# Optimization experiments

Measured on AMD Instinct MI355X. Metric: run time of the kernel, lower is better.

## Reference

```python
import jax, jax.numpy as jnp
import numpy as np

B, IN, OUT = 131072, 256, 256
BITWIDTH = 7.0


def setup_inputs() -> dict:
    key = jax.random.key(0)
    k1, k2 = jax.random.split(key)
    # simulated int8 activations (integer-valued float32)
    act_in = jax.random.randint(k1, (B, IN), -127, 128).astype(jnp.float32)
    # UniformWeights: xavier_uniform then weight_quant to the int8 grid
    limit = float(np.sqrt(6.0 / (IN + OUT)))
    w = jax.random.uniform(k2, (OUT, IN), minval=-limit, maxval=limit, dtype=jnp.float32)
    w_range = jnp.max(jnp.abs(w))
    weight_exp = (jnp.ceil(jnp.log2(w_range)) - 7.0).astype(jnp.int32)
    weight = jnp.round(w / w_range * 127.0)  # int8-valued float32 [OUT, IN]
    return {"act_in": act_in, "exp_in": jnp.int32(0), "weight": weight, "weight_exp": weight_exp}


def _round_shift(x, shift):
    # RoundShift: floor-div by 2**shift, add floor(|remainder| / 2**(shift-1)), clip to int8
    two_s = jnp.exp2(shift)
    rt = jnp.floor(x / two_s)
    prob = jnp.abs(x - rt * two_s)
    dec = jnp.floor(prob / jnp.exp2(shift - 1.0))
    return jnp.clip(rt + dec, -127.0, 127.0)


def reference(act_in, exp_in, weight, weight_exp):
    # int8 GEMM simulated in fp32 (exact: |acc| < 2^24)
    temp = act_in @ weight.T  # [B, OUT] int32 accumulator values
    # RangeEstimate: full-tensor abs-max -> bitwidth
    r = jnp.max(jnp.abs(temp))
    bw = jnp.where(r > 0, jnp.ceil(jnp.log2(jnp.maximum(r, 1.0))), 0.0)
    shift = bw - BITWIDTH
    pos = shift > 0
    safe_shift = jnp.maximum(shift, 1.0)
    rounded = _round_shift(temp, safe_shift)
    act_out = jnp.where(pos, rounded, temp).astype(jnp.int8)
    exp_sum = jnp.asarray(exp_in, jnp.int32) + jnp.asarray(weight_exp, jnp.int32)
    exp_out = (exp_sum + jnp.where(pos, shift, 0.0).astype(jnp.int32)).astype(jnp.int16)
    return act_out, exp_out
```

## Files before the change

### kernel.cpp

```cpp
#include <hip/hip_runtime.h>
#include <stdint.h>


#define M_ROWS 131072
#define NK 256
#define BM 64
#define BK 64
#define BKP 72

typedef __attribute__((ext_vector_type(8))) short bf16x8;
typedef __attribute__((ext_vector_type(4))) float f32x4;
typedef __attribute__((ext_vector_type(4))) float fv4;
typedef __attribute__((ext_vector_type(4))) int iv4;
typedef __attribute__((ext_vector_type(4))) unsigned int u32x4;
typedef __attribute__((ext_vector_type(4))) unsigned short us4;

__device__ __forceinline__ uint32_t pack_bf16(float a, float b) {
  return (__float_as_uint(a) >> 16) | (__float_as_uint(b) & 0xFFFF0000u);
}

__global__ void wconv(const float* __restrict__ w, unsigned short* __restrict__ wb,
                      int* __restrict__ gmax) {
  if (blockIdx.x == 0 && threadIdx.x == 0) *gmax = 0;
  const int i = blockIdx.x * 256 + threadIdx.x;
  const fv4 f = ((const fv4*)w)[i];
  us4 o;
  o.x = (unsigned short)(__float_as_uint(f.x) >> 16);
  o.y = (unsigned short)(__float_as_uint(f.y) >> 16);
  o.z = (unsigned short)(__float_as_uint(f.z) >> 16);
  o.w = (unsigned short)(__float_as_uint(f.w) >> 16);
  ((us4*)wb)[i] = o;
}

__device__ __forceinline__ void gemm_tile(
    const float* __restrict__ act, const unsigned short* __restrict__ wgtb,
    short* As, short* Bs, f32x4 acc[4][4])
{
  const int tid  = threadIdx.x;
  const int bm   = blockIdx.x * BM;
  const int lane = tid & 63;
  const int wave = tid >> 6;
  const int lm   = lane & 15;
  const int lk   = lane >> 4;
  const int wn   = wave * 64;

  const int arow = tid >> 3, aks = (tid & 7) * 8;
  const int brow = tid >> 3, bks = (tid & 7) * 8;

  uint32_t apk[2][4];
  u32x4 breg[8];

#pragma unroll
  for (int j = 0; j < 2; ++j) {
    const float* p = act + (size_t)(bm + arow + j * 32) * NK + aks;
    const fv4 f0 = *(const fv4*)p;
    const fv4 f1 = *((const fv4*)p + 1);
    apk[j][0] = pack_bf16(f0.x, f0.y); apk[j][1] = pack_bf16(f0.z, f0.w);
    apk[j][2] = pack_bf16(f1.x, f1.y); apk[j][3] = pack_bf16(f1.z, f1.w);
  }
#pragma unroll
  for (int j = 0; j < 8; ++j)
    breg[j] = *(const u32x4*)(wgtb + (size_t)(brow + j * 32) * NK + bks);

  for (int kt = 0; kt < NK; kt += BK) {
    __syncthreads();
#pragma unroll
    for (int j = 0; j < 2; ++j)
      *(u32x4*)&As[(arow + j * 32) * BKP + aks] = *(const u32x4*)apk[j];
#pragma unroll
    for (int j = 0; j < 8; ++j)
      *(u32x4*)&Bs[(brow + j * 32) * BKP + bks] = breg[j];
    __syncthreads();

    if (kt + BK < NK) {
      const int ktn = kt + BK;
#pragma unroll
      for (int j = 0; j < 2; ++j) {
        const float* p = act + (size_t)(bm + arow + j * 32) * NK + ktn + aks;
        const fv4 f0 = *(const fv4*)p;
        const fv4 f1 = *((const fv4*)p + 1);
        apk[j][0] = pack_bf16(f0.x, f0.y); apk[j][1] = pack_bf16(f0.z, f0.w);
        apk[j][2] = pack_bf16(f1.x, f1.y); apk[j][3] = pack_bf16(f1.z, f1.w);
      }
#pragma unroll
      for (int j = 0; j < 8; ++j)
        breg[j] = *(const u32x4*)(wgtb + (size_t)(brow + j * 32) * NK + ktn + bks);
    }

#pragma unroll
    for (int kk = 0; kk < BK; kk += 32) {
      bf16x8 af[4], bfr[4];
#pragma unroll
      for (int mi = 0; mi < 4; ++mi)
        af[mi] = *(const bf16x8*)&As[(mi * 16 + lm) * BKP + kk + lk * 8];
#pragma unroll
      for (int ni = 0; ni < 4; ++ni)
        bfr[ni] = *(const bf16x8*)&Bs[(wn + ni * 16 + lm) * BKP + kk + lk * 8];
#pragma unroll
      for (int mi = 0; mi < 4; ++mi)
#pragma unroll
        for (int ni = 0; ni < 4; ++ni)
          acc[mi][ni] = __builtin_amdgcn_mfma_f32_16x16x32_bf16(
              af[mi], bfr[ni], acc[mi][ni], 0, 0, 0);
    }
  }
}

__global__ __launch_bounds__(256, 3) void gemm_maxstore(
    const float* __restrict__ act, const unsigned short* __restrict__ wgtb,
    int* __restrict__ out, int* __restrict__ gmax)
{
  __shared__ __align__(16) short As[BM * BKP];
  __shared__ __align__(16) short Bs[NK * BKP];
  __shared__ int smax;
  const int tid = threadIdx.x;
  if (tid == 0) smax = 0;

  f32x4 acc[4][4] = {};
  gemm_tile(act, wgtb, As, Bs, acc);

  const int bm   = blockIdx.x * BM;
  const int lane = tid & 63;
  const int lm   = lane & 15;
  const int lk   = lane >> 4;
  const int wn   = (tid >> 6) * 64;

  int imax = 0;
#pragma unroll
  for (int mi = 0; mi < 4; ++mi)
#pragma unroll
    for (int ni = 0; ni < 4; ++ni)
#pragma unroll
      for (int r = 0; r < 4; ++r) {
        const int ti = (int)acc[mi][ni][r];
        const int a = ti < 0 ? -ti : ti;
        imax = a > imax ? a : imax;
        const int m = bm + mi * 16 + lk * 4 + r;
        const int n = wn + ni * 16 + lm;
        out[(size_t)m * NK + n] = ti;
      }
#pragma unroll
  for (int off = 32; off; off >>= 1) {
    const int o = __shfl_xor(imax, off, 64);
    imax = o > imax ? o : imax;
  }
  if ((tid & 63) == 0) atomicMax(&smax, imax);
  __syncthreads();
  if (tid == 0) atomicMax(gmax, smax);
}

__global__ __launch_bounds__(256) void quant_pass(
    int* __restrict__ out, const int* __restrict__ gmax,
    const int* __restrict__ exp_in, const int* __restrict__ wexp)
{
  const int rmax = *gmax;
  const int bw = (rmax <= 1) ? 0 : (32 - __clz(rmax - 1));
  const int shift = bw - 7;
  const bool pos = shift > 0;
  const int s = shift < 1 ? 1 : shift;

  const size_t total  = (size_t)M_ROWS * NK / 4;
  const size_t stride = (size_t)gridDim.x * blockDim.x;
  for (size_t i = (size_t)blockIdx.x * blockDim.x + threadIdx.x; i < total;
       i += stride) {
    iv4 t = ((const iv4*)out)[i];
    iv4 q;
#pragma unroll
    for (int j = 0; j < 4; ++j) {
      const int ti = t[j];
      int r;
      if (pos) {
        const int rt = ti >> s;
        const int dec = (ti - (rt << s)) >> (s - 1);
        r = rt + dec;
        r = r > 127 ? 127 : (r < -127 ? -127 : r);
      } else {
        r = (int)(signed char)(ti & 0xFF);
      }
      q[j] = r;
    }
    __builtin_nontemporal_store(q, &((iv4*)out)[i]);
  }

  if (blockIdx.x == 0 && threadIdx.x == 0) {
    const int e = exp_in[0] + wexp[0] + (pos ? shift : 0);
    out[(size_t)M_ROWS * NK] = (int)(short)e;
  }
}

extern "C" void kernel_launch(void* const* d_in, const int* in_sizes, int n_in,
                              void* d_out, int out_size, void* d_ws, size_t ws_size,
                              hipStream_t stream) {
  const float* act   = (const float*)d_in[0];
  const int* exp_in  = (const int*)d_in[1];
  const float* wgt   = (const float*)d_in[2];
  const int* wexp    = (const int*)d_in[3];
  int* gmax          = (int*)d_ws;
  unsigned short* wb = (unsigned short*)((char*)d_ws + 128);

  wconv<<<dim3(64), dim3(256), 0, stream>>>(wgt, wb, gmax);
  gemm_maxstore<<<dim3(M_ROWS / BM), dim3(256), 0, stream>>>(act, wb, (int*)d_out,
                                                             gmax);
  quant_pass<<<dim3(2048), dim3(256), 0, stream>>>((int*)d_out, gmax, exp_in, wexp);
}
```

Measured before the change: 280.2 us.

## Keep full weight matrix resident in LDS, stream activations directly into registers

The GEMM kernel now loads the entire bf16 weight matrix into shared memory once per block and uses 512-row blocks of 512 threads. Each wave computes 16-row strips over all 256 output columns, loading activation fragments straight from global memory into registers without staging them in LDS. This removes the per-k-tile barriers and the repeated weight staging of the old 64-row tiling. The bf16 packing now uses a byte-permute instruction, and the abs-max is tracked in float. The cost is roughly 135KB of LDS per block, which limits occupancy, plus many live registers (16 accumulators and 16 raw activation vectors).

```diff
diff --git a/kernel.cpp b/kernel.cpp
--- a/kernel.cpp
+++ b/kernel.cpp
@@ -4,9 +4,8 @@
 
 #define M_ROWS 131072
 #define NK 256
-#define BM 64
-#define BK 64
-#define BKP 72
+#define BLK_ROWS 512
+#define BST 264
 
 typedef __attribute__((ext_vector_type(8))) short bf16x8;
 typedef __attribute__((ext_vector_type(4))) float f32x4;
@@ -15,8 +14,9 @@
 typedef __attribute__((ext_vector_type(4))) unsigned int u32x4;
 typedef __attribute__((ext_vector_type(4))) unsigned short us4;
 
-__device__ __forceinline__ uint32_t pack_bf16(float a, float b) {
-  return (__float_as_uint(a) >> 16) | (__float_as_uint(b) & 0xFFFF0000u);
+__device__ __forceinline__ uint32_t pack2(float lo, float hi) {
+  return __builtin_amdgcn_perm(__float_as_uint(hi), __float_as_uint(lo),
+                               0x07060302u);
 }
 
 __global__ void wconv(const float* __restrict__ w, unsigned short* __restrict__ wb,
@@ -32,119 +32,75 @@
   ((us4*)wb)[i] = o;
 }
 
-__device__ __forceinline__ void gemm_tile(
+__global__ __launch_bounds__(512, 2) void gemm_maxstore(
     const float* __restrict__ act, const unsigned short* __restrict__ wgtb,
-    short* As, short* Bs, f32x4 acc[4][4])
+    int* __restrict__ out, int* __restrict__ gmax)
 {
-  const int tid  = threadIdx.x;
-  const int bm   = blockIdx.x * BM;
+  __shared__ __align__(16) short Bs[NK * BST];
+  __shared__ int smax;
+  const int tid = threadIdx.x;
+  if (tid == 0) smax = 0;
+
+  for (int v = tid; v < NK * NK / 8; v += 512) {
+    const int col = v >> 5;
+    const int k   = (v & 31) << 3;
+    *(u32x4*)&Bs[col * BST + k] = ((const u32x4*)wgtb)[v];
+  }
+  __syncthreads();
+
   const int lane = tid & 63;
   const int wave = tid >> 6;
   const int lm   = lane & 15;
   const int lk   = lane >> 4;
-  const int wn   = wave * 64;
+  const int bm   = blockIdx.x * BLK_ROWS;
 
-  const int arow = tid >> 3, aks = (tid & 7) * 8;
-  const int brow = tid >> 3, bks = (tid & 7) * 8;
+  float fmaxv = 0.0f;
 
-  uint32_t apk[2][4];
-  u32x4 breg[8];
+#pragma unroll 1
+  for (int s = wave; s < BLK_ROWS / 16; s += 8) {
+    const int row0 = bm + s * 16;
+    const float* arow = act + (size_t)(row0 + lm) * NK;
+
+    fv4 araw[16];
+#pragma unroll
+    for (int kk = 0; kk < 8; ++kk) {
+      araw[2 * kk]     = *(const fv4*)(arow + kk * 32 + lk * 8);
+      araw[2 * kk + 1] = *(const fv4*)(arow + kk * 32 + lk * 8 + 4);
+    }
+
+    f32x4 acc[16] = {};
+#pragma unroll
+    for (int kk = 0; kk < 8; ++kk) {
+      u32x4 apk;
+      apk.x = pack2(araw[2 * kk].x,     araw[2 * kk].y);
+      apk.y = pack2(araw[2 * kk].z,     araw[2 * kk].w);
+      apk.z = pack2(araw[2 * kk + 1].x, araw[2 * kk + 1].y);
+      apk.w = pack2(araw[2 * kk + 1].z, araw[2 * kk + 1].w);
+      const bf16x8 af = __builtin_bit_cast(bf16x8, apk);
+#pragma unroll
+      for (int ni = 0; ni < 16; ++ni) {
+        const bf16x8 bfr =
+            *(const bf16x8*)&Bs[(ni * 16 + lm) * BST + kk * 32 + lk * 8];
+        acc[ni] = __builtin_amdgcn_mfma_f32_16x16x32_bf16(af, bfr, acc[ni],
+                                                          0, 0, 0);
+      }
+    }
+
+    const size_t obase = (size_t)(row0 + lk * 4) * NK + lm;
+#pragma unroll
+    for (int ni = 0; ni < 16; ++ni)
+#pragma unroll
+      for (int r = 0; r < 4; ++r) {
+        const float tv = acc[ni][r];
+        fmaxv = fmaxf(fmaxv, fabsf(tv));
+        out[obase + (size_t)r * NK + ni * 16] = (int)tv;
+      }
+  }
 
 #pragma unroll
-  for (int j = 0; j < 2; ++j) {
-    const float* p = act + (size_t)(bm + arow + j * 32) * NK + aks;
-    const fv4 f0 = *(const fv4*)p;
-    const fv4 f1 = *((const fv4*)p + 1);
-    apk[j][0] = pack_bf16(f0.x, f0.y); apk[j][1] = pack_bf16(f0.z, f0.w);
-    apk[j][2] = pack_bf16(f1.x, f1.y); apk[j][3] = pack_bf16(f1.z, f1.w);
-  }
-#pragma unroll
-  for (int j = 0; j < 8; ++j)
-    breg[j] = *(const u32x4*)(wgtb + (size_t)(brow + j * 32) * NK + bks);
-
-  for (int kt = 0; kt < NK; kt += BK) {
-    __syncthreads();
-#pragma unroll
-    for (int j = 0; j < 2; ++j)
-      *(u32x4*)&As[(arow + j * 32) * BKP + aks] = *(const u32x4*)apk[j];
-#pragma unroll
-    for (int j = 0; j < 8; ++j)
-      *(u32x4*)&Bs[(brow + j * 32) * BKP + bks] = breg[j];
-    __syncthreads();
-
-    if (kt + BK < NK) {
-      const int ktn = kt + BK;
-#pragma unroll
-      for (int j = 0; j < 2; ++j) {
-        const float* p = act + (size_t)(bm + arow + j * 32) * NK + ktn + aks;
-        const fv4 f0 = *(const fv4*)p;
-        const fv4 f1 = *((const fv4*)p + 1);
-        apk[j][0] = pack_bf16(f0.x, f0.y); apk[j][1] = pack_bf16(f0.z, f0.w);
-        apk[j][2] = pack_bf16(f1.x, f1.y); apk[j][3] = pack_bf16(f1.z, f1.w);
-      }
-#pragma unroll
-      for (int j = 0; j < 8; ++j)
-        breg[j] = *(const u32x4*)(wgtb + (size_t)(brow + j * 32) * NK + ktn + bks);
-    }
-
-#pragma unroll
-    for (int kk = 0; kk < BK; kk += 32) {
-      bf16x8 af[4], bfr[4];
-#pragma unroll
-      for (int mi = 0; mi < 4; ++mi)
-        af[mi] = *(const bf16x8*)&As[(mi * 16 + lm) * BKP + kk + lk * 8];
-#pragma unroll
-      for (int ni = 0; ni < 4; ++ni)
-        bfr[ni] = *(const bf16x8*)&Bs[(wn + ni * 16 + lm) * BKP + kk + lk * 8];
-#pragma unroll
-      for (int mi = 0; mi < 4; ++mi)
-#pragma unroll
-        for (int ni = 0; ni < 4; ++ni)
-          acc[mi][ni] = __builtin_amdgcn_mfma_f32_16x16x32_bf16(
-              af[mi], bfr[ni], acc[mi][ni], 0, 0, 0);
-    }
-  }
-}
-
-__global__ __launch_bounds__(256, 3) void gemm_maxstore(
-    const float* __restrict__ act, const unsigned short* __restrict__ wgtb,
-    int* __restrict__ out, int* __restrict__ gmax)
-{
-  __shared__ __align__(16) short As[BM * BKP];
-  __shared__ __align__(16) short Bs[NK * BKP];
-  __shared__ int smax;
-  const int tid = threadIdx.x;
-  if (tid == 0) smax = 0;
-
-  f32x4 acc[4][4] = {};
-  gemm_tile(act, wgtb, As, Bs, acc);
-
-  const int bm   = blockIdx.x * BM;
-  const int lane = tid & 63;
-  const int lm   = lane & 15;
-  const int lk   = lane >> 4;
-  const int wn   = (tid >> 6) * 64;
-
-  int imax = 0;
-#pragma unroll
-  for (int mi = 0; mi < 4; ++mi)
-#pragma unroll
-    for (int ni = 0; ni < 4; ++ni)
-#pragma unroll
-      for (int r = 0; r < 4; ++r) {
-        const int ti = (int)acc[mi][ni][r];
-        const int a = ti < 0 ? -ti : ti;
-        imax = a > imax ? a : imax;
-        const int m = bm + mi * 16 + lk * 4 + r;
-        const int n = wn + ni * 16 + lm;
-        out[(size_t)m * NK + n] = ti;
-      }
-#pragma unroll
-  for (int off = 32; off; off >>= 1) {
-    const int o = __shfl_xor(imax, off, 64);
-    imax = o > imax ? o : imax;
-  }
-  if ((tid & 63) == 0) atomicMax(&smax, imax);
+  for (int off = 32; off; off >>= 1)
+    fmaxv = fmaxf(fmaxv, __shfl_xor(fmaxv, off, 64));
+  if (lane == 0) atomicMax(&smax, (int)fmaxv);
   __syncthreads();
   if (tid == 0) atomicMax(gmax, smax);
 }
@@ -199,7 +155,7 @@
   unsigned short* wb = (unsigned short*)((char*)d_ws + 128);
 
   wconv<<<dim3(64), dim3(256), 0, stream>>>(wgt, wb, gmax);
-  gemm_maxstore<<<dim3(M_ROWS / BM), dim3(256), 0, stream>>>(act, wb, (int*)d_out,
-                                                             gmax);
+  gemm_maxstore<<<dim3(M_ROWS / BLK_ROWS), dim3(512), 0, stream>>>(
+      act, wb, (int*)d_out, gmax);
   quant_pass<<<dim3(2048), dim3(256), 0, stream>>>((int*)d_out, gmax, exp_in, wexp);
 }
```

Result: slower. 511.5 us (+82.6%).

## Enlarge GEMM row tile to 128 with 512-thread blocks and a 2x4 wave grid

Applied to the files above, without the earlier changes.

The GEMM kernel now processes 128 rows per block with 8 waves arranged 2x4, so each block loads the full 256x256 bf16 weight tile once and shares it across twice as many rows. This halves weight reloads and staging per output row and halves the number of blocks. The bf16 packing now uses a single byte-permute instruction instead of a shift/mask/or sequence. LDS use rises with the larger A tile, and 512-thread blocks with launch bounds of 2 change occupancy.

```diff
diff --git a/kernel.cpp b/kernel.cpp
--- a/kernel.cpp
+++ b/kernel.cpp
@@ -4,7 +4,7 @@
 
 #define M_ROWS 131072
 #define NK 256
-#define BM 64
+#define BM 128
 #define BK 64
 #define BKP 72
 
@@ -16,7 +16,8 @@
 typedef __attribute__((ext_vector_type(4))) unsigned short us4;
 
 __device__ __forceinline__ uint32_t pack_bf16(float a, float b) {
-  return (__float_as_uint(a) >> 16) | (__float_as_uint(b) & 0xFFFF0000u);
+  return __builtin_amdgcn_perm(__float_as_uint(b), __float_as_uint(a),
+                               0x07060302u);
 }
 
 __global__ void wconv(const float* __restrict__ w, unsigned short* __restrict__ wb,
@@ -32,81 +33,7 @@
   ((us4*)wb)[i] = o;
 }
 
-__device__ __forceinline__ void gemm_tile(
-    const float* __restrict__ act, const unsigned short* __restrict__ wgtb,
-    short* As, short* Bs, f32x4 acc[4][4])
-{
-  const int tid  = threadIdx.x;
-  const int bm   = blockIdx.x * BM;
-  const int lane = tid & 63;
-  const int wave = tid >> 6;
-  const int lm   = lane & 15;
-  const int lk   = lane >> 4;
-  const int wn   = wave * 64;
-
-  const int arow = tid >> 3, aks = (tid & 7) * 8;
-  const int brow = tid >> 3, bks = (tid & 7) * 8;
-
-  uint32_t apk[2][4];
-  u32x4 breg[8];
-
-#pragma unroll
-  for (int j = 0; j < 2; ++j) {
-    const float* p = act + (size_t)(bm + arow + j * 32) * NK + aks;
-    const fv4 f0 = *(const fv4*)p;
-    const fv4 f1 = *((const fv4*)p + 1);
-    apk[j][0] = pack_bf16(f0.x, f0.y); apk[j][1] = pack_bf16(f0.z, f0.w);
-    apk[j][2] = pack_bf16(f1.x, f1.y); apk[j][3] = pack_bf16(f1.z, f1.w);
-  }
-#pragma unroll
-  for (int j = 0; j < 8; ++j)
-    breg[j] = *(const u32x4*)(wgtb + (size_t)(brow + j * 32) * NK + bks);
-
-  for (int kt = 0; kt < NK; kt += BK) {
-    __syncthreads();
-#pragma unroll
-    for (int j = 0; j < 2; ++j)
-      *(u32x4*)&As[(arow + j * 32) * BKP + aks] = *(const u32x4*)apk[j];
-#pragma unroll
-    for (int j = 0; j < 8; ++j)
-      *(u32x4*)&Bs[(brow + j * 32) * BKP + bks] = breg[j];
-    __syncthreads();
-
-    if (kt + BK < NK) {
-      const int ktn = kt + BK;
-#pragma unroll
-      for (int j = 0; j < 2; ++j) {
-        const float* p = act + (size_t)(bm + arow + j * 32) * NK + ktn + aks;
-        const fv4 f0 = *(const fv4*)p;
-        const fv4 f1 = *((const fv4*)p + 1);
-        apk[j][0] = pack_bf16(f0.x, f0.y); apk[j][1] = pack_bf16(f0.z, f0.w);
-        apk[j][2] = pack_bf16(f1.x, f1.y); apk[j][3] = pack_bf16(f1.z, f1.w);
-      }
-#pragma unroll
-      for (int j = 0; j < 8; ++j)
-        breg[j] = *(const u32x4*)(wgtb + (size_t)(brow + j * 32) * NK + ktn + bks);
-    }
-
-#pragma unroll
-    for (int kk = 0; kk < BK; kk += 32) {
-      bf16x8 af[4], bfr[4];
-#pragma unroll
-      for (int mi = 0; mi < 4; ++mi)
-        af[mi] = *(const bf16x8*)&As[(mi * 16 + lm) * BKP + kk + lk * 8];
-#pragma unroll
-      for (int ni = 0; ni < 4; ++ni)
-        bfr[ni] = *(const bf16x8*)&Bs[(wn + ni * 16 + lm) * BKP + kk + lk * 8];
-#pragma unroll
-      for (int mi = 0; mi < 4; ++mi)
-#pragma unroll
-        for (int ni = 0; ni < 4; ++ni)
-          acc[mi][ni] = __builtin_amdgcn_mfma_f32_16x16x32_bf16(
-              af[mi], bfr[ni], acc[mi][ni], 0, 0, 0);
-    }
-  }
-}
-
-__global__ __launch_bounds__(256, 3) void gemm_maxstore(
+__global__ __launch_bounds__(512, 2) void gemm_maxstore(
     const float* __restrict__ act, const unsigned short* __restrict__ wgtb,
     int* __restrict__ out, int* __restrict__ gmax)
 {
@@ -116,14 +43,78 @@
   const int tid = threadIdx.x;
   if (tid == 0) smax = 0;
 
-  f32x4 acc[4][4] = {};
-  gemm_tile(act, wgtb, As, Bs, acc);
-
   const int bm   = blockIdx.x * BM;
   const int lane = tid & 63;
+  const int wave = tid >> 6;
+  const int wr   = wave >> 2;
+  const int wc   = wave & 3;
   const int lm   = lane & 15;
   const int lk   = lane >> 4;
-  const int wn   = (tid >> 6) * 64;
+
+  const int arow = tid >> 3;
+  const int aks  = (tid & 7) * 8;
+  const int brow = tid >> 3;
+  const int bks  = (tid & 7) * 8;
+
+  uint32_t apk[2][4];
+  u32x4 breg[4];
+
+#pragma unroll
+  for (int j = 0; j < 2; ++j) {
+    const float* p = act + (size_t)(bm + arow + j * 64) * NK + aks;
+    const fv4 f0 = *(const fv4*)p;
+    const fv4 f1 = *((const fv4*)p + 1);
+    apk[j][0] = pack_bf16(f0.x, f0.y); apk[j][1] = pack_bf16(f0.z, f0.w);
+    apk[j][2] = pack_bf16(f1.x, f1.y); apk[j][3] = pack_bf16(f1.z, f1.w);
+  }
+#pragma unroll
+  for (int j = 0; j < 4; ++j)
+    breg[j] = *(const u32x4*)(wgtb + (size_t)(brow + j * 64) * NK + bks);
+
+  f32x4 acc[4][4] = {};
+
+  for (int kt = 0; kt < NK; kt += BK) {
+    __syncthreads();
+#pragma unroll
+    for (int j = 0; j < 2; ++j)
+      *(u32x4*)&As[(arow + j * 64) * BKP + aks] = *(const u32x4*)apk[j];
+#pragma unroll
+    for (int j = 0; j < 4; ++j)
+      *(u32x4*)&Bs[(brow + j * 64) * BKP + bks] = breg[j];
+    __syncthreads();
+
+    if (kt + BK < NK) {
+      const int ktn = kt + BK;
+#pragma unroll
+      for (int j = 0; j < 2; ++j) {
+        const float* p = act + (size_t)(bm + arow + j * 64) * NK + ktn + aks;
+        const fv4 f0 = *(const fv4*)p;
+        const fv4 f1 = *((const fv4*)p + 1);
+        apk[j][0] = pack_bf16(f0.x, f0.y); apk[j][1] = pack_bf16(f0.z, f0.w);
+        apk[j][2] = pack_bf16(f1.x, f1.y); apk[j][3] = pack_bf16(f1.z, f1.w);
+      }
+#pragma unroll
+      for (int j = 0; j < 4; ++j)
+        breg[j] = *(const u32x4*)(wgtb + (size_t)(brow + j * 64) * NK + ktn + bks);
+    }
+
+#pragma unroll
+    for (int kk = 0; kk < BK; kk += 32) {
+      bf16x8 af[4], bfr[4];
+#pragma unroll
+      for (int mi = 0; mi < 4; ++mi)
+        af[mi] = *(const bf16x8*)&As[(wr * 64 + mi * 16 + lm) * BKP + kk + lk * 8];
+#pragma unroll
+      for (int ni = 0; ni < 4; ++ni)
+        bfr[ni] = *(const bf16x8*)&Bs[(wc * 64 + ni * 16 + lm) * BKP + kk + lk * 8];
+#pragma unroll
+      for (int mi = 0; mi < 4; ++mi)
+#pragma unroll
+        for (int ni = 0; ni < 4; ++ni)
+          acc[mi][ni] = __builtin_amdgcn_mfma_f32_16x16x32_bf16(
+              af[mi], bfr[ni], acc[mi][ni], 0, 0, 0);
+    }
+  }
 
   int imax = 0;
 #pragma unroll
@@ -135,8 +126,8 @@
         const int ti = (int)acc[mi][ni][r];
         const int a = ti < 0 ? -ti : ti;
         imax = a > imax ? a : imax;
-        const int m = bm + mi * 16 + lk * 4 + r;
-        const int n = wn + ni * 16 + lm;
+        const int m = bm + wr * 64 + mi * 16 + lk * 4 + r;
+        const int n = wc * 64 + ni * 16 + lm;
         out[(size_t)m * NK + n] = ti;
       }
 #pragma unroll
@@ -144,7 +135,7 @@
     const int o = __shfl_xor(imax, off, 64);
     imax = o > imax ? o : imax;
   }
-  if ((tid & 63) == 0) atomicMax(&smax, imax);
+  if (lane == 0) atomicMax(&smax, imax);
   __syncthreads();
   if (tid == 0) atomicMax(gmax, smax);
 }
@@ -199,7 +190,7 @@
   unsigned short* wb = (unsigned short*)((char*)d_ws + 128);
 
   wconv<<<dim3(64), dim3(256), 0, stream>>>(wgt, wb, gmax);
-  gemm_maxstore<<<dim3(M_ROWS / BM), dim3(256), 0, stream>>>(act, wb, (int*)d_out,
+  gemm_maxstore<<<dim3(M_ROWS / BM), dim3(512), 0, stream>>>(act, wb, (int*)d_out,
                                                              gmax);
   quant_pass<<<dim3(2048), dim3(256), 0, stream>>>((int*)d_out, gmax, exp_in, wexp);
 }
```

New measurement: 285.8 us. 2.0% more time.
